# Kernel optimization log

Measured on AMD Instinct MI355X. Metric: run time of the kernel, lower is better.

The kernel has to match this reference:

```python
import jax, jax.numpy as jnp
import numpy as np

# ---- static config (matches init_kwargs) ----
B, N, D, FH, FW, C = 2, 6, 48, 16, 44, 80
OGH, OGW, DOWNSAMPLE = 256, 704, 16
D_MIN, D_MAX = 2.0, 58.0
XB = (-51.2, 51.2, 0.4); YB = (-51.2, 51.2, 0.4); ZB = (-10.0, 10.0, 20.0)
NX, NY, NZ = 256, 256, 1  # (ub-lb)/step per bound
DX = jnp.array([XB[2], YB[2], ZB[2]], jnp.float32)
LOWER = jnp.array([XB[0], YB[0], ZB[0]], jnp.float32)  # bx - dx/2


def _frustum():
    # UD depth discretization: d_i = d_min + i*(d_max-d_min)/D
    ds = D_MIN + (D_MAX - D_MIN) / D * np.arange(D, dtype=np.float32)
    ds = np.broadcast_to(ds[:, None, None], (D, FH, FW))
    xs = np.broadcast_to(np.linspace(0, OGW - 1, FW, dtype=np.float32)[None, None, :], (D, FH, FW))
    ys = np.broadcast_to(np.linspace(0, OGH - 1, FH, dtype=np.float32)[None, :, None], (D, FH, FW))
    return jnp.asarray(np.stack([xs, ys, ds], -1))  # [D,FH,FW,3]

FRUSTUM = _frustum()


def setup_inputs() -> dict:
    key = jax.random.key(0)
    k1, k2 = jax.random.split(key)
    x = jax.random.normal(k1, (B, N, D, FH, FW, C), dtype=jnp.float32)
    # camera-to-ego rotation: ego_x = z_cam (fwd), ego_y = -x_cam, ego_z = -y_cam
    R = np.array([[0.0, 0.0, 1.0], [-1.0, 0.0, 0.0], [0.0, -1.0, 0.0]], np.float32)
    rots = jnp.asarray(np.broadcast_to(R, (B, N, 3, 3)).copy())
    trans = 2.0 * jax.random.normal(k2, (B, N, 3), dtype=jnp.float32)
    K = np.array([[500.0, 0.0, OGW / 2.0], [0.0, 500.0, OGH / 2.0], [0.0, 0.0, 1.0]], np.float32)
    intrins = jnp.asarray(np.broadcast_to(K, (B, N, 3, 3)).copy())
    post_rots = jnp.asarray(np.broadcast_to(np.eye(3, dtype=np.float32), (B, N, 3, 3)).copy())
    post_trans = jnp.zeros((B, N, 3), jnp.float32)
    return {"x": x, "rots": rots, "trans": trans, "intrins": intrins,
            "post_rots": post_rots, "post_trans": post_trans}


def _get_geometry(rots, trans, intrins, post_rots, post_trans):
    # frustum -> ego-frame 3D points: [B,N,D,FH,FW,3]
    pts = FRUSTUM[None, None] - post_trans[:, :, None, None, None, :]
    inv_post = jnp.linalg.inv(post_rots)
    pts = jnp.einsum('bnij,bndhwj->bndhwi', inv_post, pts)
    # un-normalize pixel coords by depth
    pts = jnp.concatenate([pts[..., :2] * pts[..., 2:3], pts[..., 2:3]], axis=-1)
    combine = jnp.einsum('bnij,bnjk->bnik', rots, jnp.linalg.inv(intrins))
    pts = jnp.einsum('bnij,bndhwj->bndhwi', combine, pts)
    return pts + trans[:, :, None, None, None, :]


def _voxel_pooling(geom, x):
    Nprime = B * N * D * FH * FW
    xf = x.reshape(Nprime, C)
    # voxel indices; torch .long() truncates toward zero -> astype matches
    gi = ((geom.reshape(Nprime, 3) - LOWER) / DX).astype(jnp.int32)
    batch_ix = jnp.repeat(jnp.arange(B, dtype=jnp.int32), Nprime // B)
    kept = ((gi[:, 0] >= 0) & (gi[:, 0] < NX) &
            (gi[:, 1] >= 0) & (gi[:, 1] < NY) &
            (gi[:, 2] >= 0) & (gi[:, 2] < NZ))
    gi = jnp.where(kept[:, None], gi, 0)
    # flat index into (B, NZ, NY, NX); equivalent aggregation to sort+quickcumsum
    flat = ((batch_ix * NZ + gi[:, 2]) * NY + gi[:, 1]) * NX + gi[:, 0]
    xm = jnp.where(kept[:, None], xf, 0.0)
    pooled = jax.ops.segment_sum(xm, flat, num_segments=B * NZ * NY * NX)
    final = pooled.reshape(B, NZ, NY, NX, C).transpose(0, 4, 1, 2, 3)
    return final  # [B, C, NZ, NY, NX]


def reference(x, rots, trans, intrins, post_rots, post_trans):
    geom = _get_geometry(rots, trans, intrins, post_rots, post_trans)
    return _voxel_pooling(geom, x)
```

## Files before the change

kernel.cpp:

```cpp
#include <hip/hip_runtime.h>
#include <hip/hip_bf16.h>


#define NCH       80
#define GRID_HW   65536
#define OUT_PER_B 5242880
#define HSTRIDE   3520
#define PTS_PER_BN 33792
#define S_FLOATS  10485760
#define S_BYTES   41943040

__device__ inline void inv3(const double a[9], double inv[9]) {
    double c00 =  a[4]*a[8] - a[5]*a[7];
    double c01 = -(a[3]*a[8] - a[5]*a[6]);
    double c02 =  a[3]*a[7] - a[4]*a[6];
    double det = a[0]*c00 + a[1]*c01 + a[2]*c02;
    double id  = 1.0/det;
    inv[0] = c00*id;
    inv[1] = (a[2]*a[7]-a[1]*a[8])*id;
    inv[2] = (a[1]*a[5]-a[2]*a[4])*id;
    inv[3] = c01*id;
    inv[4] = (a[0]*a[8]-a[2]*a[6])*id;
    inv[5] = (a[2]*a[3]-a[0]*a[5])*id;
    inv[6] = c02*id;
    inv[7] = (a[1]*a[6]-a[0]*a[7])*id;
    inv[8] = (a[0]*a[4]-a[1]*a[3])*id;
}

__global__ void prep_kernel(const float* __restrict__ rots,
                            const float* __restrict__ trans,
                            const float* __restrict__ intrins,
                            const float* __restrict__ post_rots,
                            const float* __restrict__ post_trans,
                            double* __restrict__ tw) {
    int bn = threadIdx.x;
    if (bn >= 12) return;
    double pr[9], kk[9], rt[9], ipr[9], ik[9];
    #pragma unroll
    for (int i = 0; i < 9; i++) {
        pr[i] = (double)post_rots[bn*9 + i];
        kk[i] = (double)intrins[bn*9 + i];
        rt[i] = (double)rots[bn*9 + i];
    }
    inv3(pr, ipr);
    inv3(kk, ik);
    double* o = tw + bn*24;
    #pragma unroll
    for (int i = 0; i < 9; i++) o[i] = ipr[i];
    #pragma unroll
    for (int r = 0; r < 3; r++)
        #pragma unroll
        for (int c = 0; c < 3; c++)
            o[9 + r*3 + c] = rt[r*3+0]*ik[0*3+c] + rt[r*3+1]*ik[1*3+c] + rt[r*3+2]*ik[2*3+c];
    #pragma unroll
    for (int i = 0; i < 3; i++) o[18 + i] = (double)post_trans[bn*3 + i];
    #pragma unroll
    for (int i = 0; i < 3; i++) o[21 + i] = (double)trans[bn*3 + i];
}

__global__ __launch_bounds__(256) void zero_kernel(float4* __restrict__ p, int n4) {
    int i = blockIdx.x * 256 + threadIdx.x;
    int stride = gridDim.x * 256;
    for (; i < n4; i += stride) p[i] = make_float4(0.f, 0.f, 0.f, 0.f);
}

__device__ inline void geom_phase(const double* __restrict__ ws,
                                  int bn, int d, int tid,
                                  int* s_base, int* s_colbase,
                                  unsigned* s_mask, unsigned* s_fb) {
    const int b = bn / 6;
    const double* t = ws + bn * 24;
    const float dsv = __fadd_rn(2.0f, __fmul_rn((float)(56.0 / 48.0), (float)d));

    for (int idx = tid; idx < 704; idx += 256) {
        const int h = idx / 44;
        const int w = idx - h * 44;
        float xsv = (w == 43) ? 703.0f : (float)((double)w * (703.0 / 43.0));
        float ysv = (float)(h * 17);

        double px = (double)xsv - t[18];
        double py = (double)ysv - t[19];
        double pz = (double)dsv - t[20];
        double q0 = t[0]*px + t[1]*py + t[2]*pz;
        double q1 = t[3]*px + t[4]*py + t[5]*pz;
        double q2 = t[6]*px + t[7]*py + t[8]*pz;
        q0 *= q2;
        q1 *= q2;
        double e0 = t[9]*q0  + t[10]*q1 + t[11]*q2 + t[21];
        double e1 = t[12]*q0 + t[13]*q1 + t[14]*q2 + t[22];
        double e2 = t[15]*q0 + t[16]*q1 + t[17]*q2 + t[23];

        const double lxy = (double)(-51.2f);
        const double dxy = (double)(0.4f);
        int gx = (int)((e0 - lxy) / dxy);
        int gy = (int)((e1 - lxy) / dxy);
        int gz = (int)((e2 - (double)(-10.0f)) / (double)(20.0f));
        int base = -1;
        if (gx >= 0 && gx < 256 && gy >= 0 && gy < 256 && gz == 0)
            base = (b << 16) | (gy << 8) | gx;
        s_base[idx] = base;
    }
    __syncthreads();

    if (tid < 44) {
        int cb = -1; unsigned mm = 0, fb = 0;
        #pragma unroll
        for (int h = 0; h < 16; h++) {
            int pb = s_base[h * 44 + tid];
            if (pb >= 0) {
                if (cb < 0) cb = pb;
                if (pb == cb) mm |= (1u << h);
                else          fb |= (1u << h);
            }
        }
        s_colbase[tid] = cb;
        s_mask[tid]    = mm;
        s_fb[tid]      = fb;
    }
    __syncthreads();
}

__global__ __launch_bounds__(256) void scatter_grid_kernel(const float* __restrict__ x,
                                                           const double* __restrict__ ws,
                                                           float* __restrict__ S) {
    __shared__ int      s_base[704];
    __shared__ int      s_colbase[44];
    __shared__ unsigned s_mask[44];
    __shared__ unsigned s_fb[44];

    const int tid = threadIdx.x;
    const int bn  = blockIdx.x / 48;
    const int d   = blockIdx.x - bn * 48;
    geom_phase(ws, bn, d, tid, s_base, s_colbase, s_mask, s_fb);

    const float* xb0 = x + ((size_t)bn * PTS_PER_BN + (size_t)d * 704) * NCH;
    #pragma unroll
    for (int pass = 0; pass < 4; pass++) {
        int item = pass * 256 + tid;
        if (item >= 880) break;
        int w  = item / 20;
        int c4 = item - w * 20;
        unsigned mm = s_mask[w];
        unsigned fb = s_fb[w];
        if (!(mm | fb)) continue;
        const float* xb = xb0 + (size_t)w * NCH + c4 * 4;
        float ax = 0.f, ay = 0.f, az = 0.f, aw = 0.f;
        #pragma unroll
        for (int h = 0; h < 16; h++) {
            if ((mm >> h) & 1u) {
                float4 v = *(const float4*)(xb + h * HSTRIDE);
                ax += v.x; ay += v.y; az += v.z; aw += v.w;
            } else if ((fb >> h) & 1u) {
                float4 v = *(const float4*)(xb + h * HSTRIDE);
                float* sp = S + (size_t)s_base[h * 44 + w] * NCH + c4 * 4;
                atomicAdd(sp + 0, v.x);
                atomicAdd(sp + 1, v.y);
                atomicAdd(sp + 2, v.z);
                atomicAdd(sp + 3, v.w);
            }
        }
        if (mm) {
            float* sp = S + (size_t)s_colbase[w] * NCH + c4 * 4;
            atomicAdd(sp + 0, ax);
            atomicAdd(sp + 1, ay);
            atomicAdd(sp + 2, az);
            atomicAdd(sp + 3, aw);
        }
    }
}

__global__ __launch_bounds__(256) void transpose_kernel(const float* __restrict__ S,
                                                        float* __restrict__ out) {
    __shared__ float tile[64 * 81];
    const int tid = threadIdx.x;
    const int b   = blockIdx.x >> 10;
    const int v0  = (blockIdx.x & 1023) * 64;
    const float* src = S + ((size_t)(b << 16) + v0) * NCH;
    #pragma unroll
    for (int i = 0; i < 20; i++) {
        int j = i * 256 + tid;
        int v = j / 80;
        int c = j - v * 80;
        tile[v * 81 + c] = src[j];
    }
    __syncthreads();
    float* dst = out + (size_t)b * OUT_PER_B + v0;
    #pragma unroll
    for (int i = 0; i < 20; i++) {
        int k  = i * 256 + tid;
        int c  = k >> 6;
        int lv = k & 63;
        dst[(size_t)c * GRID_HW + lv] = tile[lv * 81 + c];
    }
}

__global__ __launch_bounds__(256) void scatter_direct_kernel(const float* __restrict__ x,
                                                             const double* __restrict__ ws,
                                                             float* __restrict__ out) {
    __shared__ int      s_base[704];
    __shared__ int      s_colbase[44];
    __shared__ unsigned s_mask[44];
    __shared__ unsigned s_fb[44];

    const int tid = threadIdx.x;
    const int bn  = blockIdx.x / 48;
    const int d   = blockIdx.x - bn * 48;
    geom_phase(ws, bn, d, tid, s_base, s_colbase, s_mask, s_fb);

    const float* xb0 = x + ((size_t)bn * PTS_PER_BN + (size_t)d * 704) * NCH;
    #pragma unroll
    for (int pass = 0; pass < 4; pass++) {
        int item = pass * 256 + tid;
        if (item >= 880) break;
        int w  = item / 20;
        int c4 = item - w * 20;
        unsigned mm = s_mask[w];
        unsigned fb = s_fb[w];
        if (!(mm | fb)) continue;
        const float* xb = xb0 + (size_t)w * NCH + c4 * 4;
        float ax = 0.f, ay = 0.f, az = 0.f, aw = 0.f;
        #pragma unroll
        for (int h = 0; h < 16; h++) {
            if ((mm >> h) & 1u) {
                float4 v = *(const float4*)(xb + h * HSTRIDE);
                ax += v.x; ay += v.y; az += v.z; aw += v.w;
            } else if ((fb >> h) & 1u) {
                float4 v = *(const float4*)(xb + h * HSTRIDE);
                int vb = s_base[h * 44 + w];
                float* o = out + (size_t)(vb >> 16) * OUT_PER_B + (vb & 65535);
                atomicAdd(o + (size_t)(c4*4 + 0) * GRID_HW, v.x);
                atomicAdd(o + (size_t)(c4*4 + 1) * GRID_HW, v.y);
                atomicAdd(o + (size_t)(c4*4 + 2) * GRID_HW, v.z);
                atomicAdd(o + (size_t)(c4*4 + 3) * GRID_HW, v.w);
            }
        }
        if (mm) {
            int vb = s_colbase[w];
            float* o = out + (size_t)(vb >> 16) * OUT_PER_B + (vb & 65535);
            atomicAdd(o + (size_t)(c4*4 + 0) * GRID_HW, ax);
            atomicAdd(o + (size_t)(c4*4 + 1) * GRID_HW, ay);
            atomicAdd(o + (size_t)(c4*4 + 2) * GRID_HW, az);
            atomicAdd(o + (size_t)(c4*4 + 3) * GRID_HW, aw);
        }
    }
}

extern "C" void kernel_launch(void* const* d_in, const int* in_sizes, int n_in,
                              void* d_out, int out_size, void* d_ws, size_t ws_size,
                              hipStream_t stream) {
    const float* x          = (const float*)d_in[0];
    const float* rots       = (const float*)d_in[1];
    const float* trans      = (const float*)d_in[2];
    const float* intrins    = (const float*)d_in[3];
    const float* post_rots  = (const float*)d_in[4];
    const float* post_trans = (const float*)d_in[5];
    float* out = (float*)d_out;

    if (ws_size >= (size_t)S_BYTES + 4096) {
        float*  S  = (float*)d_ws;
        double* tw = (double*)((char*)d_ws + S_BYTES);
        zero_kernel<<<2560, 256, 0, stream>>>((float4*)S, S_FLOATS / 4);
        prep_kernel<<<1, 64, 0, stream>>>(rots, trans, intrins, post_rots, post_trans, tw);
        scatter_grid_kernel<<<576, 256, 0, stream>>>(x, tw, S);
        transpose_kernel<<<2048, 256, 0, stream>>>(S, out);
    } else {
        double* tw = (double*)d_ws;
        zero_kernel<<<2560, 256, 0, stream>>>((float4*)out, out_size / 4);
        prep_kernel<<<1, 64, 0, stream>>>(rots, trans, intrins, post_rots, post_trans, tw);
        scatter_direct_kernel<<<576, 256, 0, stream>>>(x, tw, out);
    }
}
```

Measured before the change: 238.1 us.

## Split scatter blocks over half-height rows and restructure loads row-major

```diff
diff --git a/kernel.cpp b/kernel.cpp
--- a/kernel.cpp
+++ b/kernel.cpp
@@ -64,44 +64,170 @@
     for (; i < n4; i += stride) p[i] = make_float4(0.f, 0.f, 0.f, 0.f);
 }
 
-__device__ inline void geom_phase(const double* __restrict__ ws,
-                                  int bn, int d, int tid,
-                                  int* s_base, int* s_colbase,
-                                  unsigned* s_mask, unsigned* s_fb) {
-    const int b = bn / 6;
+__device__ inline int voxel_of(const double* t, int b, int d, int h, int w) {
+    float xsv = (w == 43) ? 703.0f : (float)((double)w * (703.0 / 43.0));
+    float ysv = (float)(h * 17);
+    float dsv = __fadd_rn(2.0f, __fmul_rn((float)(56.0 / 48.0), (float)d));
+
+    double px = (double)xsv - t[18];
+    double py = (double)ysv - t[19];
+    double pz = (double)dsv - t[20];
+    double q0 = t[0]*px + t[1]*py + t[2]*pz;
+    double q1 = t[3]*px + t[4]*py + t[5]*pz;
+    double q2 = t[6]*px + t[7]*py + t[8]*pz;
+    q0 *= q2;
+    q1 *= q2;
+    double e0 = t[9]*q0  + t[10]*q1 + t[11]*q2 + t[21];
+    double e1 = t[12]*q0 + t[13]*q1 + t[14]*q2 + t[22];
+    double e2 = t[15]*q0 + t[16]*q1 + t[17]*q2 + t[23];
+
+    const double lxy = (double)(-51.2f);
+    const double dxy = (double)(0.4f);
+    int gx = (int)((e0 - lxy) / dxy);
+    int gy = (int)((e1 - lxy) / dxy);
+    int gz = (int)((e2 - (double)(-10.0f)) / (double)(20.0f));
+    if (gx >= 0 && gx < 256 && gy >= 0 && gy < 256 && gz == 0)
+        return (b << 16) | (gy << 8) | gx;
+    return -1;
+}
+
+__global__ __launch_bounds__(256) void scatter_grid_kernel(const float* __restrict__ x,
+                                                           const double* __restrict__ ws,
+                                                           float* __restrict__ S) {
+    __shared__ int      s_base[8 * 44];
+    __shared__ int      s_colbase[44];
+    __shared__ unsigned s_mask[44];
+    __shared__ unsigned s_fb[44];
+
+    const int tid   = threadIdx.x;
+    const int bid   = blockIdx.x;
+    const int bn    = bid / 96;
+    const int rem   = bid - bn * 96;
+    const int d     = rem >> 1;
+    const int h0    = (rem & 1) * 8;
+    const int b     = bn / 6;
     const double* t = ws + bn * 24;
-    const float dsv = __fadd_rn(2.0f, __fmul_rn((float)(56.0 / 48.0), (float)d));
+
+    for (int idx = tid; idx < 352; idx += 256) {
+        const int hl = idx / 44;
+        const int w  = idx - hl * 44;
+        s_base[idx] = voxel_of(t, b, d, h0 + hl, w);
+    }
+    __syncthreads();
+
+    if (tid < 44) {
+        int cb = -1; unsigned mm = 0, fb = 0;
+        #pragma unroll
+        for (int hl = 0; hl < 8; hl++) {
+            int pb = s_base[hl * 44 + tid];
+            if (pb >= 0) {
+                if (cb < 0) cb = pb;
+                if (pb == cb) mm |= (1u << hl);
+                else          fb |= (1u << hl);
+            }
+        }
+        s_colbase[tid] = (cb >= 0) ? cb : 0;
+        s_mask[tid]    = mm;
+        s_fb[tid]      = fb;
+    }
+    __syncthreads();
+
+    unsigned mmk[4], fbk[4];
+    int wk[4], c4k[4], cbk[4];
+    #pragma unroll
+    for (int k = 0; k < 4; k++) {
+        const bool val = (k < 3) || (tid < 112);
+        const int  j   = val ? (k * 256 + tid) : tid;
+        const int  w   = j / 20;
+        wk[k]  = w;
+        c4k[k] = j - w * 20;
+        mmk[k] = val ? s_mask[w] : 0u;
+        fbk[k] = val ? s_fb[w]   : 0u;
+        cbk[k] = s_colbase[w];
+    }
+
+    float4 acc[4];
+    #pragma unroll
+    for (int k = 0; k < 4; k++) acc[k] = make_float4(0.f, 0.f, 0.f, 0.f);
+
+    const float* xb0 = x + ((size_t)bn * PTS_PER_BN + (size_t)d * 704 + (size_t)h0 * 44) * NCH;
+    for (int hl = 0; hl < 8; hl++) {
+        const float4* row = (const float4*)(xb0 + (size_t)hl * HSTRIDE);
+        #pragma unroll
+        for (int k = 0; k < 4; k++) {
+            const int j = wk[k] * 20 + c4k[k];
+            if ((mmk[k] >> hl) & 1u) {
+                float4 v = row[j];
+                acc[k].x += v.x; acc[k].y += v.y; acc[k].z += v.z; acc[k].w += v.w;
+            } else if ((fbk[k] >> hl) & 1u) {
+                float4 v = row[j];
+                int vb = s_base[hl * 44 + wk[k]];
+                float* sp = S + (size_t)vb * NCH + c4k[k] * 4;
+                atomicAdd(sp + 0, v.x);
+                atomicAdd(sp + 1, v.y);
+                atomicAdd(sp + 2, v.z);
+                atomicAdd(sp + 3, v.w);
+            }
+        }
+    }
+
+    #pragma unroll
+    for (int k = 0; k < 4; k++) {
+        if (mmk[k]) {
+            float* sp = S + (size_t)cbk[k] * NCH + c4k[k] * 4;
+            atomicAdd(sp + 0, acc[k].x);
+            atomicAdd(sp + 1, acc[k].y);
+            atomicAdd(sp + 2, acc[k].z);
+            atomicAdd(sp + 3, acc[k].w);
+        }
+    }
+}
+
+__global__ __launch_bounds__(256) void transpose_kernel(const float* __restrict__ S,
+                                                        float* __restrict__ out) {
+    __shared__ float tile[64 * 81];
+    const int tid = threadIdx.x;
+    const int b   = blockIdx.x >> 10;
+    const int v0  = (blockIdx.x & 1023) * 64;
+    const float* src = S + ((size_t)(b << 16) + v0) * NCH;
+    #pragma unroll
+    for (int i = 0; i < 20; i++) {
+        int j = i * 256 + tid;
+        int v = j / 80;
+        int c = j - v * 80;
+        tile[v * 81 + c] = src[j];
+    }
+    __syncthreads();
+    float* dst = out + (size_t)b * OUT_PER_B + v0;
+    #pragma unroll
+    for (int i = 0; i < 20; i++) {
+        int k  = i * 256 + tid;
+        int c  = k >> 6;
+        int lv = k & 63;
+        dst[(size_t)c * GRID_HW + lv] = tile[lv * 81 + c];
+    }
+}
+
+__global__ __launch_bounds__(256) void scatter_direct_kernel(const float* __restrict__ x,
+                                                             const double* __restrict__ ws,
+                                                             float* __restrict__ out) {
+    __shared__ int      s_base[704];
+    __shared__ int      s_colbase[44];
+    __shared__ unsigned s_mask[44];
+    __shared__ unsigned s_fb[44];
+
+    const int tid = threadIdx.x;
+    const int bn  = blockIdx.x / 48;
+    const int d   = blockIdx.x - bn * 48;
+    const int b   = bn / 6;
+    const double* t = ws + bn * 24;
 
     for (int idx = tid; idx < 704; idx += 256) {
         const int h = idx / 44;
         const int w = idx - h * 44;
-        float xsv = (w == 43) ? 703.0f : (float)((double)w * (703.0 / 43.0));
-        float ysv = (float)(h * 17);
-
-        double px = (double)xsv - t[18];
-        double py = (double)ysv - t[19];
-        double pz = (double)dsv - t[20];
-        double q0 = t[0]*px + t[1]*py + t[2]*pz;
-        double q1 = t[3]*px + t[4]*py + t[5]*pz;
-        double q2 = t[6]*px + t[7]*py + t[8]*pz;
-        q0 *= q2;
-        q1 *= q2;
-        double e0 = t[9]*q0  + t[10]*q1 + t[11]*q2 + t[21];
-        double e1 = t[12]*q0 + t[13]*q1 + t[14]*q2 + t[22];
-        double e2 = t[15]*q0 + t[16]*q1 + t[17]*q2 + t[23];
-
-        const double lxy = (double)(-51.2f);
-        const double dxy = (double)(0.4f);
-        int gx = (int)((e0 - lxy) / dxy);
-        int gy = (int)((e1 - lxy) / dxy);
-        int gz = (int)((e2 - (double)(-10.0f)) / (double)(20.0f));
-        int base = -1;
-        if (gx >= 0 && gx < 256 && gy >= 0 && gy < 256 && gz == 0)
-            base = (b << 16) | (gy << 8) | gx;
-        s_base[idx] = base;
-    }
-    __syncthreads();
-
+        s_base[idx] = voxel_of(t, b, d, h, w);
+    }
+    __syncthreads();
     if (tid < 44) {
         int cb = -1; unsigned mm = 0, fb = 0;
         #pragma unroll
@@ -113,28 +239,13 @@
                 else          fb |= (1u << h);
             }
         }
-        s_colbase[tid] = cb;
+        s_colbase[tid] = (cb >= 0) ? cb : 0;
         s_mask[tid]    = mm;
         s_fb[tid]      = fb;
     }
     __syncthreads();
-}
-
-__global__ __launch_bounds__(256) void scatter_grid_kernel(const float* __restrict__ x,
-                                                           const double* __restrict__ ws,
-                                                           float* __restrict__ S) {
-    __shared__ int      s_base[704];
-    __shared__ int      s_colbase[44];
-    __shared__ unsigned s_mask[44];
-    __shared__ unsigned s_fb[44];
-
-    const int tid = threadIdx.x;
-    const int bn  = blockIdx.x / 48;
-    const int d   = blockIdx.x - bn * 48;
-    geom_phase(ws, bn, d, tid, s_base, s_colbase, s_mask, s_fb);
 
     const float* xb0 = x + ((size_t)bn * PTS_PER_BN + (size_t)d * 704) * NCH;
-    #pragma unroll
     for (int pass = 0; pass < 4; pass++) {
         int item = pass * 256 + tid;
         if (item >= 880) break;
@@ -145,81 +256,6 @@
         if (!(mm | fb)) continue;
         const float* xb = xb0 + (size_t)w * NCH + c4 * 4;
         float ax = 0.f, ay = 0.f, az = 0.f, aw = 0.f;
-        #pragma unroll
-        for (int h = 0; h < 16; h++) {
-            if ((mm >> h) & 1u) {
-                float4 v = *(const float4*)(xb + h * HSTRIDE);
-                ax += v.x; ay += v.y; az += v.z; aw += v.w;
-            } else if ((fb >> h) & 1u) {
-                float4 v = *(const float4*)(xb + h * HSTRIDE);
-                float* sp = S + (size_t)s_base[h * 44 + w] * NCH + c4 * 4;
-                atomicAdd(sp + 0, v.x);
-                atomicAdd(sp + 1, v.y);
-                atomicAdd(sp + 2, v.z);
-                atomicAdd(sp + 3, v.w);
-            }
-        }
-        if (mm) {
-            float* sp = S + (size_t)s_colbase[w] * NCH + c4 * 4;
-            atomicAdd(sp + 0, ax);
-            atomicAdd(sp + 1, ay);
-            atomicAdd(sp + 2, az);
-            atomicAdd(sp + 3, aw);
-        }
-    }
-}
-
-__global__ __launch_bounds__(256) void transpose_kernel(const float* __restrict__ S,
-                                                        float* __restrict__ out) {
-    __shared__ float tile[64 * 81];
-    const int tid = threadIdx.x;
-    const int b   = blockIdx.x >> 10;
-    const int v0  = (blockIdx.x & 1023) * 64;
-    const float* src = S + ((size_t)(b << 16) + v0) * NCH;
-    #pragma unroll
-    for (int i = 0; i < 20; i++) {
-        int j = i * 256 + tid;
-        int v = j / 80;
-        int c = j - v * 80;
-        tile[v * 81 + c] = src[j];
-    }
-    __syncthreads();
-    float* dst = out + (size_t)b * OUT_PER_B + v0;
-    #pragma unroll
-    for (int i = 0; i < 20; i++) {
-        int k  = i * 256 + tid;
-        int c  = k >> 6;
-        int lv = k & 63;
-        dst[(size_t)c * GRID_HW + lv] = tile[lv * 81 + c];
-    }
-}
-
-__global__ __launch_bounds__(256) void scatter_direct_kernel(const float* __restrict__ x,
-                                                             const double* __restrict__ ws,
-                                                             float* __restrict__ out) {
-    __shared__ int      s_base[704];
-    __shared__ int      s_colbase[44];
-    __shared__ unsigned s_mask[44];
-    __shared__ unsigned s_fb[44];
-
-    const int tid = threadIdx.x;
-    const int bn  = blockIdx.x / 48;
-    const int d   = blockIdx.x - bn * 48;
-    geom_phase(ws, bn, d, tid, s_base, s_colbase, s_mask, s_fb);
-
-    const float* xb0 = x + ((size_t)bn * PTS_PER_BN + (size_t)d * 704) * NCH;
-    #pragma unroll
-    for (int pass = 0; pass < 4; pass++) {
-        int item = pass * 256 + tid;
-        if (item >= 880) break;
-        int w  = item / 20;
-        int c4 = item - w * 20;
-        unsigned mm = s_mask[w];
-        unsigned fb = s_fb[w];
-        if (!(mm | fb)) continue;
-        const float* xb = xb0 + (size_t)w * NCH + c4 * 4;
-        float ax = 0.f, ay = 0.f, az = 0.f, aw = 0.f;
-        #pragma unroll
         for (int h = 0; h < 16; h++) {
             if ((mm >> h) & 1u) {
                 float4 v = *(const float4*)(xb + h * HSTRIDE);
@@ -261,7 +297,7 @@
         double* tw = (double*)((char*)d_ws + S_BYTES);
         zero_kernel<<<2560, 256, 0, stream>>>((float4*)S, S_FLOATS / 4);
         prep_kernel<<<1, 64, 0, stream>>>(rots, trans, intrins, post_rots, post_trans, tw);
-        scatter_grid_kernel<<<576, 256, 0, stream>>>(x, tw, S);
+        scatter_grid_kernel<<<1152, 256, 0, stream>>>(x, tw, S);
         transpose_kernel<<<2048, 256, 0, stream>>>(S, out);
     } else {
         double* tw = (double*)d_ws;
```

Result: slower. 261.3 us (+9.8%).
